# Kernel tuning notes

Hardware: AMD Instinct MI355X
Metric: run time of the kernel (lower is better)

## Reference

```python
import jax, jax.numpy as jnp
import numpy as np

B, T = 64, 512
V, E = 512, 128      # dsl vocab, embedding dim
IMG = 1024           # img_repr_size
H = 512              # dsl_hidden_dim
A = 512              # n_actions
PAD = 0


def setup_inputs() -> dict:
    key = jax.random.key(0)
    ks = jax.random.split(key, 10)
    x1 = jax.random.normal(ks[0], (B, IMG), dtype=jnp.float32)
    x2 = jax.random.randint(ks[1], (B, T), 0, V)
    x2_lens = jax.random.randint(ks[2], (B,), 1, T + 1)
    s_in = 1.0 / np.sqrt(E + IMG)
    s_h = 1.0 / np.sqrt(H)
    emb = jax.random.normal(ks[3], (V, E), dtype=jnp.float32)
    emb = emb.at[PAD].set(0.0)  # padding_idx row is zero
    W_ih = jax.random.uniform(ks[4], (4 * H, E + IMG), jnp.float32, -s_h, s_h)
    W_hh = jax.random.uniform(ks[5], (4 * H, H), jnp.float32, -s_h, s_h)
    b_ih = jax.random.uniform(ks[6], (4 * H,), jnp.float32, -s_h, s_h)
    b_hh = jax.random.uniform(ks[7], (4 * H,), jnp.float32, -s_h, s_h)
    W_act = jax.random.uniform(ks[8], (A, H), jnp.float32, -s_h, s_h)
    b_act = jax.random.uniform(ks[9], (A,), jnp.float32, -s_h, s_h)
    return {"x1": x1, "x2": x2, "x2_lens": x2_lens, "emb": emb,
            "W_ih": W_ih, "W_hh": W_hh, "b_ih": b_ih, "b_hh": b_hh,
            "W_act": W_act, "b_act": b_act}


def reference(x1, x2, x2_lens, emb, W_ih, W_hh, b_ih, b_hh, W_act, b_act):
    # embed tokens and concat image repr at every timestep: [B, T, IMG+E]
    tok = emb[x2]                                        # [B, T, E]
    img = jnp.broadcast_to(x1[:, None, :], (B, T, IMG))  # [B, T, IMG]
    x = jnp.concatenate([img, tok], axis=2)              # [B, T, IMG+E]

    # precompute input-to-gate projections in one big GEMM
    gx = jnp.einsum('bti,gi->tbg', x, W_ih) + b_ih       # [T, B, 4H]

    def step(carry, gx_t):
        h, c = carry
        g = gx_t + h @ W_hh.T + b_hh                     # [B, 4H]
        i, f, gg, o = jnp.split(g, 4, axis=1)            # torch gate order i,f,g,o
        i = jax.nn.sigmoid(i); f = jax.nn.sigmoid(f)
        gg = jnp.tanh(gg); o = jax.nn.sigmoid(o)
        c = f * c + i * gg
        h = o * jnp.tanh(c)
        return (h, c), h

    h0 = jnp.zeros((B, H), jnp.float32)
    c0 = jnp.zeros((B, H), jnp.float32)
    (_, _), hs = jax.lax.scan(step, (h0, c0), gx)        # hs: [T, B, H]

    # hn = hidden state at each sequence's true last step (packed-seq semantics)
    idx = (x2_lens - 1).astype(jnp.int32)                # [B]
    hn = jnp.take_along_axis(hs.transpose(1, 0, 2), idx[:, None, None], axis=1)[:, 0, :]  # [B, H]

    nt = hn @ W_act.T + b_act                            # [B, A]
    return nt
```

## Files before the change

### kernel.cpp

```cpp
#include <hip/hip_runtime.h>
#include <cstdint>
#include <cstddef>


typedef _Float16     f16x8 __attribute__((ext_vector_type(8)));
typedef _Float16     f16x2 __attribute__((ext_vector_type(2)));
typedef float        f32x4 __attribute__((ext_vector_type(4)));
typedef float        f32x2 __attribute__((ext_vector_type(2)));
typedef unsigned int u32x4 __attribute__((ext_vector_type(4)));

#define TPB 256
#define NWG 64

#define WS_GX0   0
#define WS_P     524288
#define WS_HN    4718592
#define WS_HBUF  4849664
#define WS_FLAGS 4980736

__device__ __forceinline__ float sigm_(float x) { return 1.f / (1.f + __expf(-x)); }
__device__ __forceinline__ float tanh_(float x) {
    const float e = __expf(-2.f * fabsf(x));
    return copysignf((1.f - e) / (1.f + e), x);
}

__device__ __forceinline__ void st_ic_u32(unsigned int* p, unsigned int v) {
    __hip_atomic_store(p, v, __ATOMIC_RELAXED, __HIP_MEMORY_SCOPE_AGENT);
}
__device__ __forceinline__ unsigned int ld_ic_u32(const unsigned int* p) {
    return __hip_atomic_load(p, __ATOMIC_RELAXED, __HIP_MEMORY_SCOPE_AGENT);
}

__global__ void gemm_nt_bias(const float* __restrict__ A, int lda,
                             const float* __restrict__ B, int ldb,
                             float* __restrict__ C, int ldc, int K,
                             const float* __restrict__ bias1,
                             const float* __restrict__ bias2)
{
    __shared__ float As[32 * 68];
    __shared__ float Bs[32 * 68];
    const int tid = threadIdx.x;
    const int m0 = blockIdx.y * 64, n0 = blockIdx.x * 64;
    const int kchunk = K / gridDim.z;
    const int kbeg = blockIdx.z * kchunk, kend = kbeg + kchunk;
    const int tr = tid >> 4, tc = tid & 15;
    float acc[4][4] = {};

    for (int k0 = kbeg; k0 < kend; k0 += 32) {
        __syncthreads();
        #pragma unroll
        for (int idx = tid; idx < 2048; idx += TPB) {
            const int r = idx >> 5, kk = idx & 31;
            As[kk * 68 + r] = A[(size_t)(m0 + r) * lda + k0 + kk];
            Bs[kk * 68 + r] = B[(size_t)(n0 + r) * ldb + k0 + kk];
        }
        __syncthreads();
        #pragma unroll
        for (int kk = 0; kk < 32; ++kk) {
            const f32x4 a = *(const f32x4*)&As[kk * 68 + tr * 4];
            const f32x4 b = *(const f32x4*)&Bs[kk * 68 + tc * 4];
            #pragma unroll
            for (int i = 0; i < 4; ++i)
                #pragma unroll
                for (int j = 0; j < 4; ++j)
                    acc[i][j] = fmaf(a[i], b[j], acc[i][j]);
        }
    }

    const bool split = (gridDim.z > 1);
    #pragma unroll
    for (int i = 0; i < 4; ++i) {
        const int m = m0 + tr * 4 + i;
        #pragma unroll
        for (int j = 0; j < 4; ++j) {
            const int n = n0 + tc * 4 + j;
            float v = acc[i][j];
            if (blockIdx.z == 0) {
                if (bias1) v += bias1[n];
                if (bias2) v += bias2[n];
            }
            if (split) atomicAdd(&C[(size_t)m * ldc + n], v);
            else       C[(size_t)m * ldc + n] = v;
        }
    }
}

__global__ void __launch_bounds__(TPB, 1)
lstm_seq(const float* __restrict__ Whh,
         const float* __restrict__ GX0,
         const float* __restrict__ P,
         const int*   __restrict__ x2,
         const int*   __restrict__ lens,
         _Float16*    hbuf,
         float*       __restrict__ hn,
         unsigned int* flags)
{
    __shared__ float Spart[4 * 128 * 20];

    const int tid = threadIdx.x, wg = blockIdx.x;
    const int lane = tid & 63, wv = tid >> 6;
    const int BG = wg >> 4;
    const int CG = wg & 15;
    const int m16 = lane & 15, q = lane >> 4;

    const int bl  = tid >> 4;
    const int cq  = (tid & 15) * 2;
    const int b   = BG * 16 + bl;
    const int col = CG * 32 + cq;
    const int last = lens[b] - 1;
    const int* toks = x2 + b * 512;

    f32x2 gxv[4];
    {
        const float* gx = GX0 + (size_t)b * 2048 + col;
        #pragma unroll
        for (int g = 0; g < 4; ++g) gxv[g] = *(const f32x2*)(gx + g * 512);
    }

    { f16x2 z; z[0] = (_Float16)0.f; z[1] = (_Float16)0.f;
      st_ic_u32((unsigned int*)(hbuf + b * 512 + col),
                __builtin_bit_cast(unsigned int, z)); }
    __syncthreads();
    unsigned int* myflag = flags + (size_t)wg * 64;
    if (tid == 0) st_ic_u32(myflag, 1u);

    const unsigned int* pollp =
        flags + (size_t)(BG * 16 + wv * 4 + (lane & 3)) * 64;

    f16x8 bfr[8][4];
    #pragma unroll
    for (int n = 0; n < 8; ++n) {
        const int rr = n * 16 + m16;
        const int gr = (rr >> 5) * 512 + CG * 32 + (rr & 31);
        const float* wrow = Whh + (size_t)gr * 512 + wv * 128 + q * 8;
        #pragma unroll
        for (int ks = 0; ks < 4; ++ks) {
            const f32x4 w0 = *(const f32x4*)(wrow + ks * 32);
            const f32x4 w1 = *(const f32x4*)(wrow + ks * 32 + 4);
            f16x8 bv;
            #pragma unroll
            for (int e = 0; e < 4; ++e) {
                bv[e]     = (_Float16)w0[e];
                bv[4 + e] = (_Float16)w1[e];
            }
            bfr[n][ks] = bv;
        }
    }

    int tok1;
    f32x2 ppv[4], ppn[4];
    {
        const int tok0 = toks[0];
        const float* pp = P + (size_t)tok0 * 2048 + col;
        #pragma unroll
        for (int g = 0; g < 4; ++g) ppv[g] = *(const f32x2*)(pp + g * 512);
        tok1 = toks[1];
    }

    float c0 = 0.f, c1 = 0.f;

    for (int t = 0; t < 512; ++t) {
        const unsigned int tgt = (unsigned int)(t + 1);

        while (true) {
            const unsigned int v = ld_ic_u32(pollp);
            if (__all((int)(v >= tgt))) break;
        }
        asm volatile("" ::: "memory");

        const _Float16* hsrc = hbuf + (size_t)(t & 1) * (64 * 512);
        _Float16*       hdst = hbuf + (size_t)((t + 1) & 1) * (64 * 512);

        u32x4 a0, a1, a2, a3;
        {
            const _Float16* ap =
                hsrc + (BG * 16 + m16) * 512 + wv * 128 + q * 8;
            asm volatile(
                "global_load_dwordx4 %0, %4, off sc1\n\t"
                "global_load_dwordx4 %1, %4, off offset:64 sc1\n\t"
                "global_load_dwordx4 %2, %4, off offset:128 sc1\n\t"
                "global_load_dwordx4 %3, %4, off offset:192 sc1\n\t"
                "s_waitcnt vmcnt(0)"
                : "=&v"(a0), "=&v"(a1), "=&v"(a2), "=&v"(a3)
                : "v"(ap)
                : "memory");
        }
        f16x8 af[4] = {
            __builtin_bit_cast(f16x8, a0), __builtin_bit_cast(f16x8, a1),
            __builtin_bit_cast(f16x8, a2), __builtin_bit_cast(f16x8, a3)
        };

        {
            const float* ppn_ptr = P + (size_t)tok1 * 2048 + col;
            #pragma unroll
            for (int g = 0; g < 4; ++g)
                ppn[g] = *(const f32x2*)(ppn_ptr + g * 512);
            tok1 = toks[t < 510 ? t + 2 : 511];
        }

        f32x4 acc[8] = {};
        #pragma unroll
        for (int ks = 0; ks < 4; ++ks)
            #pragma unroll
            for (int n = 0; n < 8; ++n)
                acc[n] = __builtin_amdgcn_mfma_f32_16x16x32_f16(
                    af[ks], bfr[n][ks], acc[n], 0, 0, 0);

        {
            const int cl = lane & 15, r0 = (lane >> 4) * 4;
            #pragma unroll
            for (int n = 0; n < 8; ++n)
                *(f32x4*)&Spart[(wv * 128 + n * 16 + cl) * 20 + r0] = acc[n];
        }
        __syncthreads();

        f32x2 sv[4];
        #pragma unroll
        for (int g = 0; g < 4; ++g) {
            f32x2 s = {0.f, 0.f};
            #pragma unroll
            for (int w = 0; w < 4; ++w) {
                const int base = (w * 128 + g * 32 + cq) * 20 + bl;
                s[0] += Spart[base];
                s[1] += Spart[base + 20];
            }
            sv[g] = s;
        }

        float hv[2];
        #pragma unroll
        for (int p = 0; p < 2; ++p) {
            const float iv = sigm_(sv[0][p] + gxv[0][p] + ppv[0][p]);
            const float fv = sigm_(sv[1][p] + gxv[1][p] + ppv[1][p]);
            const float gv = tanh_(sv[2][p] + gxv[2][p] + ppv[2][p]);
            const float ov = sigm_(sv[3][p] + gxv[3][p] + ppv[3][p]);
            float& c = p ? c1 : c0;
            c = fv * c + iv * gv;
            hv[p] = ov * tanh_(c);
        }

        f16x2 hh; hh[0] = (_Float16)hv[0]; hh[1] = (_Float16)hv[1];
        st_ic_u32((unsigned int*)(hdst + b * 512 + col),
                  __builtin_bit_cast(unsigned int, hh));
        if (t == last) {
            f32x2 o; o[0] = hv[0]; o[1] = hv[1];
            *(f32x2*)(hn + (size_t)b * 512 + col) = o;
        }

        __syncthreads();
        if (tid == 0) st_ic_u32(myflag, (unsigned int)(t + 2));

        #pragma unroll
        for (int g = 0; g < 4; ++g) ppv[g] = ppn[g];
    }
}

extern "C" void kernel_launch(void* const* d_in, const int* in_sizes, int n_in,
                              void* d_out, int out_size, void* d_ws, size_t ws_size,
                              hipStream_t stream)
{
    const float* x1    = (const float*)d_in[0];
    const int*   x2    = (const int*)  d_in[1];
    const int*   lens  = (const int*)  d_in[2];
    const float* emb   = (const float*)d_in[3];
    const float* W_ih  = (const float*)d_in[4];
    const float* W_hh  = (const float*)d_in[5];
    const float* b_ih  = (const float*)d_in[6];
    const float* b_hh  = (const float*)d_in[7];
    const float* W_act = (const float*)d_in[8];
    const float* b_act = (const float*)d_in[9];
    float* out = (float*)d_out;

    char* ws = (char*)d_ws;
    float*        GX0   = (float*)(ws + WS_GX0);
    float*        P     = (float*)(ws + WS_P);
    float*        hn    = (float*)(ws + WS_HN);
    _Float16*     hbuf  = (_Float16*)(ws + WS_HBUF);
    unsigned int* flags = (unsigned int*)(ws + WS_FLAGS);

    hipMemsetAsync(flags, 0, 16384, stream);
    hipMemsetAsync(GX0, 0, 64 * 2048 * sizeof(float), stream);
    hipMemsetAsync(out, 0, 64 * 512 * sizeof(float), stream);

    gemm_nt_bias<<<dim3(32, 1, 4), TPB, 0, stream>>>(
        x1, 1024, W_ih, 1152, GX0, 2048, 1024, b_ih, b_hh);
    gemm_nt_bias<<<dim3(32, 8, 1), TPB, 0, stream>>>(
        emb, 128, W_ih + 1024, 1152, P, 2048, 128, nullptr, nullptr);

    lstm_seq<<<NWG, TPB, 0, stream>>>(W_hh, GX0, P, x2, lens, hbuf, hn, flags);

    gemm_nt_bias<<<dim3(8, 1, 4), TPB, 0, stream>>>(
        hn, 512, W_act, 512, out, 512, 512, b_act, nullptr);
}
```

Baseline: 1.508 ms.

## Replace end-of-step block barrier with per-wave flags and double-buffered LDS

Drops the second __syncthreads per timestep. Each wave now publishes its own progress flag after waiting for its global stores, and pollers check 4 per-wave flags per producer workgroup. The LDS partial-sum buffer is double-buffered by timestep parity so the next step's writes cannot race the current reads. The LDS stride changes from 20 to 17 to reduce bank conflicts, at the cost of scalar rather than vector LDS stores. The trade is fewer block-wide barriers against more flag polling traffic and wider flags.

```diff
diff --git a/kernel.cpp b/kernel.cpp
--- a/kernel.cpp
+++ b/kernel.cpp
@@ -95,7 +95,7 @@
          float*       __restrict__ hn,
          unsigned int* flags)
 {
-    __shared__ float Spart[4 * 128 * 20];
+    __shared__ float Spart[2][4 * 128 * 17];
 
     const int tid = threadIdx.x, wg = blockIdx.x;
     const int lane = tid & 63, wv = tid >> 6;
@@ -120,12 +120,13 @@
     { f16x2 z; z[0] = (_Float16)0.f; z[1] = (_Float16)0.f;
       st_ic_u32((unsigned int*)(hbuf + b * 512 + col),
                 __builtin_bit_cast(unsigned int, z)); }
-    __syncthreads();
-    unsigned int* myflag = flags + (size_t)wg * 64;
-    if (tid == 0) st_ic_u32(myflag, 1u);
+    asm volatile("s_waitcnt vmcnt(0)" ::: "memory");
+    unsigned int* myflag = flags + (size_t)(wg * 4 + wv) * 16;
+    if (lane == 0) st_ic_u32(myflag, 1u);
 
     const unsigned int* pollp =
-        flags + (size_t)(BG * 16 + wv * 4 + (lane & 3)) * 64;
+        flags + (size_t)(((BG * 16 + wv * 4 + (lane & 3)) * 4
+                          + ((lane >> 2) & 3)) ) * 16;
 
     f16x8 bfr[8][4];
     #pragma unroll
@@ -206,25 +207,29 @@
                 acc[n] = __builtin_amdgcn_mfma_f32_16x16x32_f16(
                     af[ks], bfr[n][ks], acc[n], 0, 0, 0);
 
+        float* sp = &Spart[t & 1][0];
         {
             const int cl = lane & 15, r0 = (lane >> 4) * 4;
             #pragma unroll
-            for (int n = 0; n < 8; ++n)
-                *(f32x4*)&Spart[(wv * 128 + n * 16 + cl) * 20 + r0] = acc[n];
+            for (int n = 0; n < 8; ++n) {
+                const int base = (wv * 128 + n * 16 + cl) * 17 + r0;
+                #pragma unroll
+                for (int r = 0; r < 4; ++r) sp[base + r] = acc[n][r];
+            }
         }
         __syncthreads();
 
         f32x2 sv[4];
         #pragma unroll
         for (int g = 0; g < 4; ++g) {
-            f32x2 s = {0.f, 0.f};
+            float s0 = 0.f, s1 = 0.f;
             #pragma unroll
             for (int w = 0; w < 4; ++w) {
-                const int base = (w * 128 + g * 32 + cq) * 20 + bl;
-                s[0] += Spart[base];
-                s[1] += Spart[base + 20];
-            }
-            sv[g] = s;
+                const int base = (w * 128 + g * 32 + cq) * 17 + bl;
+                s0 += sp[base];
+                s1 += sp[base + 17];
+            }
+            sv[g][0] = s0; sv[g][1] = s1;
         }
 
         float hv[2];
@@ -247,8 +252,8 @@
             *(f32x2*)(hn + (size_t)b * 512 + col) = o;
         }
 
-        __syncthreads();
-        if (tid == 0) st_ic_u32(myflag, (unsigned int)(t + 2));
+        asm volatile("s_waitcnt vmcnt(0)" ::: "memory");
+        if (lane == 0) st_ic_u32(myflag, (unsigned int)(t + 2));
 
         #pragma unroll
         for (int g = 0; g < 4; ++g) ppv[g] = ppn[g];
```

Result: slower. 1.783 ms (+18.2%).
